# Kernel tuning notes

Measured on AMD Instinct MI355X. Metric: run time of the kernel, lower is better.

Reference implementation:

```python
import jax, jax.numpy as jnp
import numpy as np

N, SEQ_LEN, HORIZON, F_IN, EMBED, HIDDEN, LAYERS = 4096, 168, 24, 32, 32, 64, 2
G4 = 4 * HIDDEN
# NOTE: original torch code calls nn.LSTM per-step WITHOUT carrying hidden state,
# so each step's LSTM starts from (h0=0, c0=0): W_hh contributes nothing, only b_hh.

def setup_inputs() -> dict:
    key = jax.random.key(0)
    ks = jax.random.split(key, 12)
    s = 0.1
    return {
        "X": jax.random.normal(ks[0], (N, SEQ_LEN, F_IN), jnp.float32),
        "y": jax.random.normal(ks[1], (N, SEQ_LEN), jnp.float32),
        "Xf": jax.random.normal(ks[2], (N, HORIZON, F_IN), jnp.float32),
        "W_embed": jax.random.normal(ks[3], (EMBED, 1), jnp.float32) * s,
        "b_embed": jax.random.normal(ks[4], (EMBED,), jnp.float32) * s,
        "W_ih": jax.random.normal(ks[5], (LAYERS, G4, EMBED + F_IN), jnp.float32) * s,  # layer1 in-dim == HIDDEN == EMBED+F_IN
        "b_ih": jax.random.normal(ks[6], (LAYERS, G4), jnp.float32) * s,
        "b_hh": jax.random.normal(ks[7], (LAYERS, G4), jnp.float32) * s,
        "W_mu": jax.random.normal(ks[8], (1, HIDDEN), jnp.float32) * s,
        "b_mu": jax.random.normal(ks[9], (1,), jnp.float32) * s,
        "W_sigma": jax.random.normal(ks[10], (1, HIDDEN), jnp.float32) * s,
        "b_sigma": jax.random.normal(ks[11], (1,), jnp.float32) * s,
    }


def reference(X, y, Xf, W_embed, b_embed, W_ih, b_ih, b_hh, W_mu, b_mu, W_sigma, b_sigma):
    num_ts = X.shape[0]
    T = SEQ_LEN + HORIZON
    Xall = jnp.concatenate([X, Xf], axis=1)  # (N, T, F_IN)
    y_pad = jnp.concatenate([y, jnp.zeros((num_ts, HORIZON), y.dtype)], axis=1)  # (N, T)
    use_y = jnp.arange(T) < SEQ_LEN  # teacher-forced region

    def step(carry, inputs):
        x_s, y_s, use = inputs  # (N, F_IN), (N,), scalar bool
        ynext = jnp.where(use, y_s[:, None], carry)  # (N, 1)
        yembed = ynext @ W_embed.T + b_embed  # (N, EMBED)
        h = jnp.concatenate([x_s, yembed], axis=1)  # (N, F_IN+EMBED)
        for l in range(LAYERS):  # single LSTM step from zero state per layer
            gates = h @ W_ih[l].T + b_ih[l] + b_hh[l]  # (N, 4H); torch gate order i,f,g,o
            i_g, f_g, g_g, o_g = jnp.split(gates, 4, axis=1)
            c = jax.nn.sigmoid(i_g) * jnp.tanh(g_g)  # f * c0 term vanishes (c0 = 0)
            h = jax.nn.sigmoid(o_g) * jnp.tanh(c)
        h = jax.nn.relu(h)
        mu = h @ W_mu.T + b_mu  # (N, 1)
        sigma = jax.nn.softplus(h @ W_sigma.T + b_sigma) + 1e-6  # log(1+exp(.)) + eps
        lik = (2.0 * np.pi * sigma ** 2) ** (-0.5) * jnp.exp(-((ynext - mu) ** 2) / (2.0 * sigma ** 2))
        return lik, (lik[:, 0], mu[:, 0], sigma[:, 0])

    carry0 = jnp.zeros((num_ts, 1), X.dtype)
    xs = (jnp.swapaxes(Xall, 0, 1), y_pad.T, use_y)
    _, (lik_t, mu_t, sigma_t) = jax.lax.scan(step, carry0, xs)  # each (T, N)
    ypred = lik_t.T[:, SEQ_LEN - 1: SEQ_LEN + HORIZON - 1]  # (N, HORIZON)
    return ypred, mu_t.T, sigma_t.T
```

## Files before the change

kernel.cpp:

```cpp
#include <hip/hip_runtime.h>
#include <math.h>

#define N_TS 4096
#define SEQ  168
#define HOR  24
#define T_ALL 192
#define F_INP 32
#define HID  64
#define NROW 192
#define NB_B (N_TS / 16)
#define NT_B ((N_TS * SEQ) / 64)
#define L2E  1.44269504089f
#define W16F_L1  6144
#define W16F_L1P 18432

typedef _Float16 half8  __attribute__((ext_vector_type(8)));
typedef _Float16 half4  __attribute__((ext_vector_type(4)));
typedef float    floatx4 __attribute__((ext_vector_type(4)));

__device__ __forceinline__ float fexp(float x)  { return __expf(x); }
__device__ __forceinline__ float ex2(float x)   { return __builtin_amdgcn_exp2f(x); }
__device__ __forceinline__ float frcp(float x)  { return __builtin_amdgcn_rcpf(x); }
__device__ __forceinline__ float softplus_(float x) { return (x > 15.0f) ? x : __logf(1.0f + fexp(x)); }

__device__ __forceinline__ float lstm_h(float ip, float gp, float op) {
    const float Ei = ex2(ip);
    const float Eg = ex2(gp);
    const float cc = (1.0f - Eg) * frcp((1.0f + Ei) * (1.0f + Eg));
    const float Ec = ex2(cc * (-2.0f * L2E));
    const float Eo = ex2(op);
    return (1.0f - Ec) * frcp((1.0f + Ec) * (1.0f + Eo));
}

__device__ __forceinline__ half8 cvt8(const float4 a, const float4 b) {
    half8 v;
    v[0]=(_Float16)a.x; v[1]=(_Float16)a.y; v[2]=(_Float16)a.z; v[3]=(_Float16)a.w;
    v[4]=(_Float16)b.x; v[5]=(_Float16)b.y; v[6]=(_Float16)b.z; v[7]=(_Float16)b.w;
    return v;
}

__global__ __launch_bounds__(256) void prep(
    const float* __restrict__ W_ih, const float* __restrict__ b_ih,
    const float* __restrict__ b_hh,
    const float* __restrict__ W_embed, const float* __restrict__ b_embed,
    _Float16* __restrict__ W16f, float* __restrict__ bsum,
    float* __restrict__ wy1, float* __restrict__ b1c)
{
    const int idx = blockIdx.x * 256 + threadIdx.x;
    for (int i = idx; i < 4 * NROW * 8; i += gridDim.x * 256) {
        const int kp  = i & 7;
        const int row = (i >> 3) % NROW;
        const int kb  = (i >> 3) / NROW;
        const int sr  = (row < 64) ? row : row + 64;
        const float sc = (row >= 64 && row < 128) ? (-2.0f * L2E) : (-L2E);
        W16f[i] = (_Float16)(W_ih[sr * HID + kb * 8 + kp] * sc);
    }
    for (int i = idx; i < 8 * NROW * 8; i += gridDim.x * 256) {
        const int kp  = i & 7;
        const int row = (i >> 3) % NROW;
        const int kb  = (i >> 3) / NROW;
        const int sr  = (row < 64) ? row : row + 64;
        const float sc = (row >= 64 && row < 128) ? (-2.0f * L2E) : (-L2E);
        W16f[W16F_L1 + i] = (_Float16)(W_ih[(256 + sr) * HID + kb * 8 + kp] * sc);
    }
    for (int i = idx; i < 2 * 6144; i += gridDim.x * 256) {
        const int h    = i / 6144;
        const int rem  = i - h * 6144;
        const int kp   = rem & 7;
        const int t    = rem >> 3;
        const int rowb = t % 96;
        const int kb   = t / 96;
        const int gate = rowb >> 5;
        const int jtl  = (rowb >> 4) & 1;
        const int r16  = rowb & 15;
        const int jt   = h * 2 + jtl;
        const int srow = gate * 64 + jt * 16 + r16;
        const int sr   = (srow < 64) ? srow : srow + 64;
        const int k    = kb * 8 + kp;
        const int kk   = k & 31;
        const int d    = (kk >> 1) & 3;
        const int q    = kk >> 3;
        const int e    = kk & 1;
        const int hid  = d * 16 + q * 4 + ((k >> 5) << 1) + e;
        const float sc = (gate == 1) ? (-2.0f * L2E) : (-L2E);
        W16f[W16F_L1P + i] = (_Float16)(W_ih[(256 + sr) * HID + hid] * sc);
    }
    for (int i = idx; i < 2 * NROW; i += gridDim.x * 256) {
        const int r = i % NROW;
        const int l = i / NROW;
        const int sr = (r < 64) ? r : r + 64;
        const float sc = (r >= 64 && r < 128) ? (-2.0f * L2E) : (-L2E);
        bsum[i] = (b_ih[l * 256 + sr] + b_hh[l * 256 + sr]) * sc;
    }
    if (idx < NROW) {
        const int sr = (idx < 64) ? idx : idx + 64;
        const float sc = (idx >= 64 && idx < 128) ? (-2.0f * L2E) : (-L2E);
        const float* wrow = W_ih + sr * HID + 32;
        float s1 = 0.f, s2 = 0.f;
        #pragma unroll
        for (int k = 0; k < 32; ++k) {
            s1 = fmaf(wrow[k], W_embed[k], s1);
            s2 = fmaf(wrow[k], b_embed[k], s2);
        }
        wy1[idx] = s1 * sc;
        b1c[idx] = (b_ih[sr] + b_hh[sr] + s2) * sc;
    }
}

__global__ __launch_bounds__(256, 6) void fused(
    const float* __restrict__ X,
    const float* __restrict__ y,
    const float* __restrict__ Xf,
    const float* __restrict__ W_embed,
    const float* __restrict__ b_embed,
    const _Float16* __restrict__ W16f,
    const float* __restrict__ bsum,
    const float* __restrict__ wy1,
    const float* __restrict__ b1c,
    const float* __restrict__ W_mu,
    const float* __restrict__ b_mu,
    const float* __restrict__ W_sigma,
    const float* __restrict__ b_sigma,
    float* __restrict__ out)
{
    __shared__ union __align__(16) {
        struct { _Float16 Wl[6144]; } A;
        struct { _Float16 slab[16 * 64]; float partm[16][4]; float parts[16][4];
                 float wyb[NROW]; float b1cb[NROW]; } B;
    } sh;

    const int tid = threadIdx.x;
    float* mu_out = out + (size_t)N_TS * HOR;
    float* sg_out = mu_out + (size_t)N_TS * T_ALL;

    if (blockIdx.x < NB_B) {
        __builtin_amdgcn_s_setprio(1);
        const int w    = tid >> 6;
        const int lane = tid & 63;
        const int quad = lane >> 4;
        const int ln   = lane & 15;
        const int n0   = blockIdx.x * 16;

        if (tid < NROW) {
            sh.B.wyb[tid]  = wy1[tid];
            sh.B.b1cb[tid] = b1c[tid];
        }

        half8 B1[3];
        half8 B2[3][2];
        float bias2[3];
        #pragma unroll
        for (int j = 0; j < 3; ++j) {
            const int rt = j * 4 + w;
            B1[j] = *(const half8*)(W16f + ((size_t)quad * NROW + rt * 16 + ln) * 8);
            #pragma unroll
            for (int kt = 0; kt < 2; ++kt)
                B2[j][kt] = *(const half8*)(W16f + W16F_L1 + ((size_t)(kt * 4 + quad) * NROW + rt * 16 + ln) * 8);
            bias2[j] = bsum[NROW + rt * 16 + ln];
        }
        const float wmu = W_mu[w * 16 + ln], wsg = W_sigma[w * 16 + ln];
        const float bmu = b_mu[0], bsg = b_sigma[0];

        const float* xfp = Xf + (size_t)(n0 + ln) * HOR * F_INP + quad * 8;
        float4 xa, xb;
        {
            const float* xp = X + ((size_t)(n0 + ln) * SEQ + (SEQ - 1)) * F_INP + quad * 8;
            xa = *(const float4*)xp;
            xb = *(const float4*)(xp + 4);
        }
        float ycur = y[(size_t)(n0 + ln) * SEQ + (SEQ - 1)];
        __syncthreads();

        #pragma unroll 1
        for (int it = 0; it <= HOR + 1; ++it) {
            if (it > 0) {
                const int k = it - 1;
                const float4 m4 = *(const float4*)sh.B.partm[ln];
                const float4 s4 = *(const float4*)sh.B.parts[ln];
                const float mu = (m4.x + m4.y) + (m4.z + m4.w) + bmu;
                const float sg = softplus_((s4.x + s4.y) + (s4.z + s4.w) + bsg) + 1e-6f;
                const float d  = ycur - mu;
                const float is = frcp(sg);
                const float lik = 0.39894228040143267f * is * fexp(-0.5f * d * d * is * is);
                if (k > 0 && w == 0 && quad == 0) {
                    const int nn = n0 + ln;
                    const int t  = SEQ + k - 1;
                    mu_out[(size_t)nn * T_ALL + t] = mu;
                    sg_out[(size_t)nn * T_ALL + t] = sg;
                    if (k < HOR) out[(size_t)nn * HOR + k] = lik;
                }
                ycur = lik;
            }
            if (it > HOR) break;

            const half8 xf0 = cvt8(xa, xb);
            if (it < HOR) {
                xa = *(const float4*)(xfp + it * F_INP);
                xb = *(const float4*)(xfp + it * F_INP + 4);
            }

            floatx4 t0 = *(const floatx4*)(sh.B.b1cb + 0 * 64 + w * 16 + quad * 4);
            floatx4 t1 = *(const floatx4*)(sh.B.b1cb + 1 * 64 + w * 16 + quad * 4);
            floatx4 t2 = *(const floatx4*)(sh.B.b1cb + 2 * 64 + w * 16 + quad * 4);
            t0 = __builtin_amdgcn_mfma_f32_16x16x32_f16(B1[0], xf0, t0, 0, 0, 0);
            t1 = __builtin_amdgcn_mfma_f32_16x16x32_f16(B1[1], xf0, t1, 0, 0, 0);
            t2 = __builtin_amdgcn_mfma_f32_16x16x32_f16(B1[2], xf0, t2, 0, 0, 0);

            const floatx4 wy0  = *(const floatx4*)(sh.B.wyb + 0 * 64 + w * 16 + quad * 4);
            const floatx4 wy1v = *(const floatx4*)(sh.B.wyb + 1 * 64 + w * 16 + quad * 4);
            const floatx4 wy2  = *(const floatx4*)(sh.B.wyb + 2 * 64 + w * 16 + quad * 4);

            half4 h1p;
            #pragma unroll
            for (int r = 0; r < 4; ++r) {
                const float ig = fmaf(ycur, wy0[r],  t0[r]);
                const float gg = fmaf(ycur, wy1v[r], t1[r]);
                const float og = fmaf(ycur, wy2[r],  t2[r]);
                h1p[r] = (_Float16)lstm_h(ig, gg, og);
            }
            {
                const int xblk = (2 * w + (quad >> 1)) ^ (ln & 7);
                *(half4*)(&sh.B.slab[ln * 64 + xblk * 8 + (quad & 1) * 4]) = h1p;
            }
            __syncthreads();

            const half8 a0 = *(const half8*)(&sh.B.slab[ln * 64 + ((quad ^ (ln & 7)) << 3)]);
            const half8 a1 = *(const half8*)(&sh.B.slab[ln * 64 + (((4 + quad) ^ (ln & 7)) << 3)]);
            floatx4 acc[3];
            #pragma unroll
            for (int j = 0; j < 3; ++j) {
                acc[j] = (floatx4){bias2[j], bias2[j], bias2[j], bias2[j]};
                acc[j] = __builtin_amdgcn_mfma_f32_16x16x32_f16(a0, B2[j][0], acc[j], 0, 0, 0);
                acc[j] = __builtin_amdgcn_mfma_f32_16x16x32_f16(a1, B2[j][1], acc[j], 0, 0, 0);
            }

            float pmr[4], psr[4];
            #pragma unroll
            for (int r = 0; r < 4; ++r) {
                const float hh = lstm_h(acc[0][r], acc[1][r], acc[2][r]);
                const float hr = fmaxf(hh, 0.0f);
                pmr[r] = hr * wmu;
                psr[r] = hr * wsg;
            }
            #pragma unroll
            for (int off = 1; off < 16; off <<= 1) {
                #pragma unroll
                for (int r = 0; r < 4; ++r) {
                    pmr[r] += __shfl_xor(pmr[r], off, 64);
                    psr[r] += __shfl_xor(psr[r], off, 64);
                }
            }
            if (ln == 0) {
                #pragma unroll
                for (int r = 0; r < 4; ++r) {
                    sh.B.partm[quad * 4 + r][w] = pmr[r];
                    sh.B.parts[quad * 4 + r][w] = psr[r];
                }
            }
            __syncthreads();
        }
        return;
    }

    const int w    = tid >> 6;
    const int lane = tid & 63;
    const int quad = lane >> 4;
    const int ln   = lane & 15;
    const int cid  = (blockIdx.x - NB_B) * 64 + w * 16 + ln;

    half8 xfr;
    {
        const float* xp = X + (size_t)cid * F_INP + quad * 8;
        xfr = cvt8(*(const float4*)xp, *(const float4*)(xp + 4));
    }
    const float yv = y[cid];

    #pragma unroll
    for (int c = 0; c < 3; ++c) {
        const int off = (c * 256 + tid) * 8;
        *(half8*)(sh.A.Wl + off) = *(const half8*)(W16f + off);
    }
    __syncthreads();

    half8 a0, a1;
    {
        const _Float16* bp = sh.A.Wl + quad * 1536 + ln * 8;
        #pragma unroll
        for (int jt = 0; jt < 4; ++jt) {
            floatx4 ai = *(const floatx4*)(b1c + jt * 16 + quad * 4);
            floatx4 ag = *(const floatx4*)(b1c + 64 + jt * 16 + quad * 4);
            floatx4 ao = *(const floatx4*)(b1c + 128 + jt * 16 + quad * 4);
            ai = __builtin_amdgcn_mfma_f32_16x16x32_f16(*(const half8*)(bp + jt * 128),        xfr, ai, 0, 0, 0);
            ag = __builtin_amdgcn_mfma_f32_16x16x32_f16(*(const half8*)(bp + 512 + jt * 128),  xfr, ag, 0, 0, 0);
            ao = __builtin_amdgcn_mfma_f32_16x16x32_f16(*(const half8*)(bp + 1024 + jt * 128), xfr, ao, 0, 0, 0);
            const floatx4 wyi = *(const floatx4*)(wy1 + jt * 16 + quad * 4);
            const floatx4 wyg = *(const floatx4*)(wy1 + 64 + jt * 16 + quad * 4);
            const floatx4 wyo = *(const floatx4*)(wy1 + 128 + jt * 16 + quad * 4);
            a0[2 * jt + 0] = (_Float16)lstm_h(fmaf(yv, wyi[0], ai[0]),
                                              fmaf(yv, wyg[0], ag[0]),
                                              fmaf(yv, wyo[0], ao[0]));
            a0[2 * jt + 1] = (_Float16)lstm_h(fmaf(yv, wyi[1], ai[1]),
                                              fmaf(yv, wyg[1], ag[1]),
                                              fmaf(yv, wyo[1], ao[1]));
            a1[2 * jt + 0] = (_Float16)lstm_h(fmaf(yv, wyi[2], ai[2]),
                                              fmaf(yv, wyg[2], ag[2]),
                                              fmaf(yv, wyo[2], ao[2]));
            a1[2 * jt + 1] = (_Float16)lstm_h(fmaf(yv, wyi[3], ai[3]),
                                              fmaf(yv, wyg[3], ag[3]),
                                              fmaf(yv, wyo[3], ao[3]));
        }
    }
    __syncthreads();

    float pm = 0.f, ps = 0.f;
    #pragma unroll
    for (int h = 0; h < 2; ++h) {
        #pragma unroll
        for (int c = 0; c < 3; ++c) {
            const int off = (c * 256 + tid) * 8;
            *(half8*)(sh.A.Wl + off) = *(const half8*)(W16f + W16F_L1P + h * 6144 + off);
        }
        __syncthreads();
        const _Float16* bp = sh.A.Wl + quad * 768 + ln * 8;
        #pragma unroll
        for (int jtl = 0; jtl < 2; ++jtl) {
            const int jt = h * 2 + jtl;
            floatx4 ai = *(const floatx4*)(bsum + NROW + jt * 16 + quad * 4);
            floatx4 ag = *(const floatx4*)(bsum + NROW + 64 + jt * 16 + quad * 4);
            floatx4 ao = *(const floatx4*)(bsum + NROW + 128 + jt * 16 + quad * 4);
            ai = __builtin_amdgcn_mfma_f32_16x16x32_f16(*(const half8*)(bp + jtl * 128),               a0, ai, 0, 0, 0);
            ai = __builtin_amdgcn_mfma_f32_16x16x32_f16(*(const half8*)(bp + jtl * 128 + 3072),        a1, ai, 0, 0, 0);
            ag = __builtin_amdgcn_mfma_f32_16x16x32_f16(*(const half8*)(bp + 256 + jtl * 128),         a0, ag, 0, 0, 0);
            ag = __builtin_amdgcn_mfma_f32_16x16x32_f16(*(const half8*)(bp + 256 + jtl * 128 + 3072),  a1, ag, 0, 0, 0);
            ao = __builtin_amdgcn_mfma_f32_16x16x32_f16(*(const half8*)(bp + 512 + jtl * 128),         a0, ao, 0, 0, 0);
            ao = __builtin_amdgcn_mfma_f32_16x16x32_f16(*(const half8*)(bp + 512 + jtl * 128 + 3072),  a1, ao, 0, 0, 0);
            const floatx4 wm  = *(const floatx4*)(W_mu + jt * 16 + quad * 4);
            const floatx4 ws4 = *(const floatx4*)(W_sigma + jt * 16 + quad * 4);
            #pragma unroll
            for (int r = 0; r < 4; ++r) {
                const float hr = fmaxf(lstm_h(ai[r], ag[r], ao[r]), 0.0f);
                pm = fmaf(hr, wm[r], pm);
                ps = fmaf(hr, ws4[r], ps);
            }
        }
        __syncthreads();
    }

    pm += __shfl_xor(pm, 16, 64); pm += __shfl_xor(pm, 32, 64);
    ps += __shfl_xor(ps, 16, 64); ps += __shfl_xor(ps, 32, 64);

    if (quad == 0) {
        const int n = cid / SEQ;
        const int t = cid - n * SEQ;
        const float mu = pm + b_mu[0];
        const float sg = softplus_(ps + b_sigma[0]) + 1e-6f;
        mu_out[(size_t)n * T_ALL + t] = mu;
        sg_out[(size_t)n * T_ALL + t] = sg;
        if (t == SEQ - 1) {
            const float d  = yv - mu;
            const float is = frcp(sg);
            out[(size_t)n * HOR] = 0.39894228040143267f * is * fexp(-0.5f * d * d * is * is);
        }
    }
}

extern "C" void kernel_launch(void* const* d_in, const int* in_sizes, int n_in,
                              void* d_out, int out_size, void* d_ws, size_t ws_size,
                              hipStream_t stream) {
    const float* X       = (const float*)d_in[0];
    const float* y       = (const float*)d_in[1];
    const float* Xf      = (const float*)d_in[2];
    const float* W_embed = (const float*)d_in[3];
    const float* b_embed = (const float*)d_in[4];
    const float* W_ih    = (const float*)d_in[5];
    const float* b_ih    = (const float*)d_in[6];
    const float* b_hh    = (const float*)d_in[7];
    const float* W_mu    = (const float*)d_in[8];
    const float* b_mu    = (const float*)d_in[9];
    const float* W_sigma = (const float*)d_in[10];
    const float* b_sigma = (const float*)d_in[11];

    float* out = (float*)d_out;
    _Float16*  W16f = (_Float16*)d_ws;
    float*     bsum = (float*)((char*)d_ws + 61440);
    float*     wy1  = (float*)((char*)d_ws + 61440 + 1536);
    float*     b1c  = (float*)((char*)d_ws + 61440 + 1536 + 768);

    prep<<<96, 256, 0, stream>>>(W_ih, b_ih, b_hh, W_embed, b_embed,
                                 W16f, bsum, wy1, b1c);

    fused<<<NB_B + NT_B, 256, 0, stream>>>(
        X, y, Xf, W_embed, b_embed, W16f, bsum, wy1, b1c,
        W_mu, b_mu, W_sigma, b_sigma, out);
}
```

Baseline: 249.5 us.

## Keep all layer weights resident in LDS and loop four tiles per block

Teacher-forced blocks now load the layer-0 weights and both halves of the layer-1 weights into shared memory once. Each block then processes four 64-row tiles in a loop instead of one, so the grid for that path shrinks fourfold. This removes the repeated weight reloads and the barriers between layer halves. In exchange the shared-memory footprint triples to about 36 KB per block, which may reduce occupancy against the launch bound of 6 blocks. Fewer blocks also means less parallelism across CUs.

Measured after the change: 316.9 us. 27.0% more time.

```diff
diff --git a/kernel.cpp b/kernel.cpp
--- a/kernel.cpp
+++ b/kernel.cpp
@@ -9,7 +9,7 @@
 #define HID  64
 #define NROW 192
 #define NB_B (N_TS / 16)
-#define NT_B ((N_TS * SEQ) / 64)
+#define NT_B ((N_TS * SEQ) / 256)
 #define L2E  1.44269504089f
 #define W16F_L1  6144
 #define W16F_L1P 18432
@@ -124,7 +124,7 @@
     float* __restrict__ out)
 {
     __shared__ union __align__(16) {
-        struct { _Float16 Wl[6144]; } A;
+        struct { _Float16 Wl0[6144]; _Float16 Wlh[2][6144]; } A;
         struct { _Float16 slab[16 * 64]; float partm[16][4]; float parts[16][4];
                  float wyb[NROW]; float b1cb[NROW]; } B;
     } sh;
@@ -266,33 +266,39 @@
     const int lane = tid & 63;
     const int quad = lane >> 4;
     const int ln   = lane & 15;
-    const int cid  = (blockIdx.x - NB_B) * 64 + w * 16 + ln;
-
-    half8 xfr;
-    {
-        const float* xp = X + (size_t)cid * F_INP + quad * 8;
-        xfr = cvt8(*(const float4*)xp, *(const float4*)(xp + 4));
-    }
-    const float yv = y[cid];
 
     #pragma unroll
     for (int c = 0; c < 3; ++c) {
         const int off = (c * 256 + tid) * 8;
-        *(half8*)(sh.A.Wl + off) = *(const half8*)(W16f + off);
+        *(half8*)(sh.A.Wl0 + off)    = *(const half8*)(W16f + off);
+        *(half8*)(sh.A.Wlh[0] + off) = *(const half8*)(W16f + W16F_L1P + off);
+        *(half8*)(sh.A.Wlh[1] + off) = *(const half8*)(W16f + W16F_L1P + 6144 + off);
     }
     __syncthreads();
 
-    half8 a0, a1;
-    {
-        const _Float16* bp = sh.A.Wl + quad * 1536 + ln * 8;
+    const _Float16* bp0 = sh.A.Wl0 + quad * 1536 + ln * 8;
+    const int tile0 = (blockIdx.x - NB_B) * 4;
+
+    #pragma unroll 1
+    for (int tt = 0; tt < 4; ++tt) {
+        const int cid = (tile0 + tt) * 64 + w * 16 + ln;
+
+        half8 xfr;
+        {
+            const float* xp = X + (size_t)cid * F_INP + quad * 8;
+            xfr = cvt8(*(const float4*)xp, *(const float4*)(xp + 4));
+        }
+        const float yv = y[cid];
+
+        half8 a0, a1;
         #pragma unroll
         for (int jt = 0; jt < 4; ++jt) {
             floatx4 ai = *(const floatx4*)(b1c + jt * 16 + quad * 4);
             floatx4 ag = *(const floatx4*)(b1c + 64 + jt * 16 + quad * 4);
             floatx4 ao = *(const floatx4*)(b1c + 128 + jt * 16 + quad * 4);
-            ai = __builtin_amdgcn_mfma_f32_16x16x32_f16(*(const half8*)(bp + jt * 128),        xfr, ai, 0, 0, 0);
-            ag = __builtin_amdgcn_mfma_f32_16x16x32_f16(*(const half8*)(bp + 512 + jt * 128),  xfr, ag, 0, 0, 0);
-            ao = __builtin_amdgcn_mfma_f32_16x16x32_f16(*(const half8*)(bp + 1024 + jt * 128), xfr, ao, 0, 0, 0);
+            ai = __builtin_amdgcn_mfma_f32_16x16x32_f16(*(const half8*)(bp0 + jt * 128),        xfr, ai, 0, 0, 0);
+            ag = __builtin_amdgcn_mfma_f32_16x16x32_f16(*(const half8*)(bp0 + 512 + jt * 128),  xfr, ag, 0, 0, 0);
+            ao = __builtin_amdgcn_mfma_f32_16x16x32_f16(*(const half8*)(bp0 + 1024 + jt * 128), xfr, ao, 0, 0, 0);
             const floatx4 wyi = *(const floatx4*)(wy1 + jt * 16 + quad * 4);
             const floatx4 wyg = *(const floatx4*)(wy1 + 64 + jt * 16 + quad * 4);
             const floatx4 wyo = *(const floatx4*)(wy1 + 128 + jt * 16 + quad * 4);
@@ -309,57 +315,49 @@
                                               fmaf(yv, wyg[3], ag[3]),
                                               fmaf(yv, wyo[3], ao[3]));
         }
-    }
-    __syncthreads();
-
-    float pm = 0.f, ps = 0.f;
-    #pragma unroll
-    for (int h = 0; h < 2; ++h) {
+
+        float pm = 0.f, ps = 0.f;
         #pragma unroll
-        for (int c = 0; c < 3; ++c) {
-            const int off = (c * 256 + tid) * 8;
-            *(half8*)(sh.A.Wl + off) = *(const half8*)(W16f + W16F_L1P + h * 6144 + off);
-        }
-        __syncthreads();
-        const _Float16* bp = sh.A.Wl + quad * 768 + ln * 8;
-        #pragma unroll
-        for (int jtl = 0; jtl < 2; ++jtl) {
-            const int jt = h * 2 + jtl;
-            floatx4 ai = *(const floatx4*)(bsum + NROW + jt * 16 + quad * 4);
-            floatx4 ag = *(const floatx4*)(bsum + NROW + 64 + jt * 16 + quad * 4);
-            floatx4 ao = *(const floatx4*)(bsum + NROW + 128 + jt * 16 + quad * 4);
-            ai = __builtin_amdgcn_mfma_f32_16x16x32_f16(*(const half8*)(bp + jtl * 128),               a0, ai, 0, 0, 0);
-            ai = __builtin_amdgcn_mfma_f32_16x16x32_f16(*(const half8*)(bp + jtl * 128 + 3072),        a1, ai, 0, 0, 0);
-            ag = __builtin_amdgcn_mfma_f32_16x16x32_f16(*(const half8*)(bp + 256 + jtl * 128),         a0, ag, 0, 0, 0);
-            ag = __builtin_amdgcn_mfma_f32_16x16x32_f16(*(const half8*)(bp + 256 + jtl * 128 + 3072),  a1, ag, 0, 0, 0);
-            ao = __builtin_amdgcn_mfma_f32_16x16x32_f16(*(const half8*)(bp + 512 + jtl * 128),         a0, ao, 0, 0, 0);
-            ao = __builtin_amdgcn_mfma_f32_16x16x32_f16(*(const half8*)(bp + 512 + jtl * 128 + 3072),  a1, ao, 0, 0, 0);
-            const floatx4 wm  = *(const floatx4*)(W_mu + jt * 16 + quad * 4);
-            const floatx4 ws4 = *(const floatx4*)(W_sigma + jt * 16 + quad * 4);
-            #pragma unroll
-            for (int r = 0; r < 4; ++r) {
-                const float hr = fmaxf(lstm_h(ai[r], ag[r], ao[r]), 0.0f);
-                pm = fmaf(hr, wm[r], pm);
-                ps = fmaf(hr, ws4[r], ps);
-            }
-        }
-        __syncthreads();
-    }
-
-    pm += __shfl_xor(pm, 16, 64); pm += __shfl_xor(pm, 32, 64);
-    ps += __shfl_xor(ps, 16, 64); ps += __shfl_xor(ps, 32, 64);
-
-    if (quad == 0) {
-        const int n = cid / SEQ;
-        const int t = cid - n * SEQ;
-        const float mu = pm + b_mu[0];
-        const float sg = softplus_(ps + b_sigma[0]) + 1e-6f;
-        mu_out[(size_t)n * T_ALL + t] = mu;
-        sg_out[(size_t)n * T_ALL + t] = sg;
-        if (t == SEQ - 1) {
-            const float d  = yv - mu;
-            const float is = frcp(sg);
-            out[(size_t)n * HOR] = 0.39894228040143267f * is * fexp(-0.5f * d * d * is * is);
+        for (int h = 0; h < 2; ++h) {
+            const _Float16* bp = sh.A.Wlh[h] + quad * 768 + ln * 8;
+            #pragma unroll
+            for (int jtl = 0; jtl < 2; ++jtl) {
+                const int jt = h * 2 + jtl;
+                floatx4 ai = *(const floatx4*)(bsum + NROW + jt * 16 + quad * 4);
+                floatx4 ag = *(const floatx4*)(bsum + NROW + 64 + jt * 16 + quad * 4);
+                floatx4 ao = *(const floatx4*)(bsum + NROW + 128 + jt * 16 + quad * 4);
+                ai = __builtin_amdgcn_mfma_f32_16x16x32_f16(*(const half8*)(bp + jtl * 128),               a0, ai, 0, 0, 0);
+                ai = __builtin_amdgcn_mfma_f32_16x16x32_f16(*(const half8*)(bp + jtl * 128 + 3072),        a1, ai, 0, 0, 0);
+                ag = __builtin_amdgcn_mfma_f32_16x16x32_f16(*(const half8*)(bp + 256 + jtl * 128),         a0, ag, 0, 0, 0);
+                ag = __builtin_amdgcn_mfma_f32_16x16x32_f16(*(const half8*)(bp + 256 + jtl * 128 + 3072),  a1, ag, 0, 0, 0);
+                ao = __builtin_amdgcn_mfma_f32_16x16x32_f16(*(const half8*)(bp + 512 + jtl * 128),         a0, ao, 0, 0, 0);
+                ao = __builtin_amdgcn_mfma_f32_16x16x32_f16(*(const half8*)(bp + 512 + jtl * 128 + 3072),  a1, ao, 0, 0, 0);
+                const floatx4 wm  = *(const floatx4*)(W_mu + jt * 16 + quad * 4);
+                const floatx4 ws4 = *(const floatx4*)(W_sigma + jt * 16 + quad * 4);
+                #pragma unroll
+                for (int r = 0; r < 4; ++r) {
+                    const float hr = fmaxf(lstm_h(ai[r], ag[r], ao[r]), 0.0f);
+                    pm = fmaf(hr, wm[r], pm);
+                    ps = fmaf(hr, ws4[r], ps);
+                }
+            }
+        }
+
+        pm += __shfl_xor(pm, 16, 64); pm += __shfl_xor(pm, 32, 64);
+        ps += __shfl_xor(ps, 16, 64); ps += __shfl_xor(ps, 32, 64);
+
+        if (quad == 0) {
+            const int n = cid / SEQ;
+            const int t = cid - n * SEQ;
+            const float mu = pm + b_mu[0];
+            const float sg = softplus_(ps + b_sigma[0]) + 1e-6f;
+            mu_out[(size_t)n * T_ALL + t] = mu;
+            sg_out[(size_t)n * T_ALL + t] = sg;
+            if (t == SEQ - 1) {
+                const float d  = yv - mu;
+                const float is = frcp(sg);
+                out[(size_t)n * HOR] = 0.39894228040143267f * is * fexp(-0.5f * d * d * is * is);
+            }
         }
     }
 }
```
